# Kernel optimization log

Hardware: AMD Instinct MI355X
Metric: run time of the kernel (lower is better)

## Reference

```python
import jax, jax.numpy as jnp
import numpy as np

B, S, D = 8, 8192, 64
N_HASHES = 8
BUCKET_SIZE = 64
N_BUCKETS = S // BUCKET_SIZE  # 128
SELF_ATTN_VALUE = -5e4  # torch reformer TOKEN_SELF_ATTN_VALUE


def setup_inputs() -> dict:
    key = jax.random.key(0)
    k1, k2, k3 = jax.random.split(key, 3)
    qk = jax.random.normal(k1, (B, S, D), dtype=jnp.float32)
    v = jax.random.normal(k2, (B, S, D), dtype=jnp.float32)
    # LSH random rotations: (dim, n_hashes, n_buckets // 2), shared across batch/heads
    rotations = jax.random.normal(k3, (D, N_HASHES, N_BUCKETS // 2), dtype=jnp.float32)
    return {"qk": qk, "v": v, "rotations": rotations, "query_len": S}


def _look_one_back(x):
    # concatenate each chunk with the preceding chunk (wrapping) along the kv axis
    x_extra = jnp.concatenate([x[:, -1:], x[:, :-1]], axis=1)
    return jnp.concatenate([x, x_extra], axis=2)


def _lsh_bucketed_dots(qk, v, rotations):
    batch, seqlen, dim = qk.shape
    n_buckets = seqlen // BUCKET_SIZE
    # --- hash vectors: rotate, concat with negation, argmax -> bucket ids ---
    rotated = jnp.einsum('btf,fhi->bhti', qk, rotations)           # (B, H, S, nb/2)
    rotated = jnp.concatenate([rotated, -rotated], axis=-1)        # (B, H, S, nb)
    buckets = jnp.argmax(rotated, axis=-1)                         # (B, H, S) int
    offsets = (jnp.arange(N_HASHES) * n_buckets)[None, :, None]    # disjoint per round
    buckets = (buckets + offsets).reshape(batch, -1)               # (B, H*S)

    # --- stable bucket sort via composite key (all keys unique) ---
    ticker = jnp.arange(N_HASHES * seqlen)[None, :]                # (1, H*S)
    buckets_and_t = seqlen * buckets + (ticker % seqlen)
    sticker = jnp.argsort(buckets_and_t, axis=-1)                  # sort permutation
    undo_sort = jnp.argsort(sticker, axis=-1)                      # inverse permutation
    st = sticker % seqlen                                          # original token ids

    # --- gather tokens into bucket order ---
    sqk = jnp.take_along_axis(qk, st[..., None], axis=1)           # (B, H*S, D)
    sv = jnp.take_along_axis(v, st[..., None], axis=1)

    n_chunks = N_HASHES * n_buckets
    bq_t = st.reshape(batch, n_chunks, BUCKET_SIZE)                # (B, C, bs)
    bqk = sqk.reshape(batch, n_chunks, BUCKET_SIZE, dim)
    bv = sv.reshape(batch, n_chunks, BUCKET_SIZE, dim)

    bq = bqk
    bk = bqk / (jnp.linalg.norm(bqk, axis=-1, keepdims=True) + 1e-6)  # unit-length keys

    bk = _look_one_back(bk)       # (B, C, 2*bs, D)
    bv = _look_one_back(bv)
    bkv_t = _look_one_back(bq_t)  # (B, C, 2*bs)

    dots = jnp.einsum('buie,buje->buij', bq, bk) * (dim ** -0.5)   # (B, C, bs, 2*bs)
    self_mask = bq_t[:, :, :, None] == bkv_t[:, :, None, :]
    dots = jnp.where(self_mask, SELF_ATTN_VALUE, dots)
    return dots, undo_sort, bv


def reference(qk, v, rotations, query_len):
    batch, seqlen, dim = qk.shape
    dots, undo_sort, bv = _lsh_bucketed_dots(qk, v, rotations)
    dots_logsumexp = jax.nn.logsumexp(dots, axis=-1, keepdims=True)
    p = jnp.exp(dots - dots_logsumexp)                             # per-bucket softmax
    bo = jnp.einsum('buij,buje->buie', p, bv)                      # (B, C, bs, D)
    so = bo.reshape(batch, -1, dim)                                # (B, H*S, D)
    slogits = dots_logsumexp.reshape(batch, -1)                    # (B, H*S)
    # undo the bucket sort
    o = jnp.take_along_axis(so, undo_sort[..., None], axis=1)
    logits = jnp.take_along_axis(slogits, undo_sort, axis=1)
    o = o.reshape(batch, N_HASHES, seqlen, dim)[:, :, :query_len]
    logits = logits.reshape(batch, N_HASHES, seqlen, 1)[:, :, :query_len]
    # combine across hash rounds, weighted by per-round logsumexp
    probs = jnp.exp(logits - jax.nn.logsumexp(logits, axis=1, keepdims=True))
    out = jnp.sum(o * probs, axis=1)                               # (B, query_len, D)
    return out
```

## Files before the change

kernel.cpp:

```cpp
#include <hip/hip_runtime.h>
#include <math.h>

#define B_  8
#define S_  8192
#define D_  64
#define H_  8
#define NB_ 128
#define NC_ 1024
#define REP_CAP 65536
#define T2_ 2e-3f

typedef _Float16 f16x8 __attribute__((ext_vector_type(8)));
typedef _Float16 f16x2 __attribute__((ext_vector_type(2)));
typedef float    f32x4 __attribute__((ext_vector_type(4)));
typedef unsigned int uint_;

#define MFMA16(A, Bv, C) __builtin_amdgcn_mfma_f32_16x16x32_f16(A, Bv, C, 0, 0, 0)

__global__ __launch_bounds__(256) void rot_prep_kernel(
    const float* __restrict__ rot, _Float16* __restrict__ rotHi,
    _Float16* __restrict__ rotLo, float* __restrict__ rotT,
    int* __restrict__ cnt)
{
  __shared__ float rs[64 * 64];
  const int tid = threadIdx.x, h = blockIdx.x;
  if (h == 0 && tid == 0) *cnt = 0;
#pragma unroll
  for (int it = 0; it < 16; ++it) {
    const int f = it * 4 + (tid >> 6), i = tid & 63;
    rs[f * 64 + i] = rot[f * 512 + h * 64 + i];
  }
  __syncthreads();
  const int i = tid & 63, grp = tid >> 6;
  _Float16 hi[16], lo[16];
  float tf[16];
#pragma unroll
  for (int ff = 0; ff < 16; ++ff) {
    const float x = rs[(grp * 16 + ff) * 64 + i];
    tf[ff] = x;
    hi[ff] = (_Float16)x;
    lo[ff] = (_Float16)(x - (float)hi[ff]);
  }
  f16x8* dH = (f16x8*)(rotHi + h * 4096 + i * 64 + grp * 16);
  f16x8* dL = (f16x8*)(rotLo + h * 4096 + i * 64 + grp * 16);
  dH[0] = ((f16x8*)hi)[0]; dH[1] = ((f16x8*)hi)[1];
  dL[0] = ((f16x8*)lo)[0]; dL[1] = ((f16x8*)lo)[1];
  float4* dT = (float4*)(rotT + h * 4096 + i * 64 + grp * 16);
#pragma unroll
  for (int k = 0; k < 4; ++k) dT[k] = ((float4*)tf)[k];
}

__global__ __launch_bounds__(256) void hash_kernel(
    const float* __restrict__ qk, const float* __restrict__ v,
    const _Float16* __restrict__ rotHi, const _Float16* __restrict__ rotLo,
    _Float16* __restrict__ q16, _Float16* __restrict__ kn16,
    _Float16* __restrict__ v16,
    int* __restrict__ bucket, int* __restrict__ cnt, int2* __restrict__ list)
{
  __shared__ _Float16 rH[64 * 72];
  __shared__ _Float16 rL[64 * 72];
  const int tid  = threadIdx.x;
  const int b    = blockIdx.x & 7;
  const int tile = blockIdx.x >> 3;
  const int lane = tid & 63, w = tid >> 6;
  const int m16  = lane & 15, qd = lane >> 4;

  {
    const int gt = b * S_ + tile * 64 + (tid >> 2);
    const int qu = tid & 3;
    const size_t off = (size_t)gt * 64 + qu * 16;
    float x[16];
#pragma unroll
    for (int k = 0; k < 4; ++k) ((float4*)x)[k] = ((const float4*)(qk + off))[k];
    float ss = 0.f;
#pragma unroll
    for (int k = 0; k < 16; ++k) ss = fmaf(x[k], x[k], ss);
    ss += __shfl_xor(ss, 1); ss += __shfl_xor(ss, 2);
    const float inv = 0.125f / (sqrtf(ss) + 1e-6f);
    f16x8 qh[2], kn[2];
#pragma unroll
    for (int j = 0; j < 16; ++j) {
      qh[j >> 3][j & 7] = (_Float16)x[j];
      kn[j >> 3][j & 7] = (_Float16)(x[j] * inv);
    }
    ((f16x8*)(q16  + off))[0] = qh[0]; ((f16x8*)(q16  + off))[1] = qh[1];
    ((f16x8*)(kn16 + off))[0] = kn[0]; ((f16x8*)(kn16 + off))[1] = kn[1];
    float y[16];
#pragma unroll
    for (int k = 0; k < 4; ++k) ((float4*)y)[k] = ((const float4*)(v + off))[k];
    f16x8 vv[2];
#pragma unroll
    for (int j = 0; j < 16; ++j) vv[j >> 3][j & 7] = (_Float16)y[j];
    ((f16x8*)(v16 + off))[0] = vv[0]; ((f16x8*)(v16 + off))[1] = vv[1];
  }

  const int t = tile * 64 + w * 16 + m16;
  f16x8 BH0, BH1, BL0, BL1;
  {
    const float* src = qk + ((size_t)b * S_ + t) * 64 + 8 * qd;
    float x[16];
    ((float4*)x)[0] = ((const float4*)src)[0];
    ((float4*)x)[1] = ((const float4*)(src + 4))[0];
    ((float4*)x)[2] = ((const float4*)(src + 32))[0];
    ((float4*)x)[3] = ((const float4*)(src + 36))[0];
#pragma unroll
    for (int j = 0; j < 8; ++j) {
      const _Float16 h0 = (_Float16)x[j];
      BH0[j] = h0; BL0[j] = (_Float16)(x[j] - (float)h0);
      const _Float16 h1 = (_Float16)x[j + 8];
      BH1[j] = h1; BL1[j] = (_Float16)(x[j + 8] - (float)h1);
    }
  }
  const int srow = tid >> 2, scol = (tid & 3) * 16;
  const uint_ qd16 = (uint_)(qd << 4);

  f16x8 cH0, cH1, cL0, cL1;
  {
    const _Float16* gH = rotHi + srow * 64 + scol;
    const _Float16* gL = rotLo + srow * 64 + scol;
    cH0 = ((const f16x8*)gH)[0]; cH1 = ((const f16x8*)gH)[1];
    cL0 = ((const f16x8*)gL)[0]; cL1 = ((const f16x8*)gL)[1];
  }

#pragma unroll 1
  for (int h = 0; h < 8; ++h) {
    __syncthreads();
    f16x8 nH0, nH1, nL0, nL1;
    if (h < 7) {
      const _Float16* gH = rotHi + (h + 1) * 4096 + srow * 64 + scol;
      const _Float16* gL = rotLo + (h + 1) * 4096 + srow * 64 + scol;
      nH0 = ((const f16x8*)gH)[0]; nH1 = ((const f16x8*)gH)[1];
      nL0 = ((const f16x8*)gL)[0]; nL1 = ((const f16x8*)gL)[1];
    }
    *(f16x8*)(rH + srow * 72 + scol)     = cH0;
    *(f16x8*)(rH + srow * 72 + scol + 8) = cH1;
    *(f16x8*)(rL + srow * 72 + scol)     = cL0;
    *(f16x8*)(rL + srow * 72 + scol + 8) = cL1;
    __syncthreads();

    f32x4 acc[4];
#pragma unroll
    for (int mt = 0; mt < 4; ++mt) acc[mt] = (f32x4){0.f, 0.f, 0.f, 0.f};
#pragma unroll
    for (int mt = 0; mt < 4; ++mt) {
      const _Float16* aH = rH + (16 * mt + m16) * 72 + 8 * qd;
      const _Float16* aL = rL + (16 * mt + m16) * 72 + 8 * qd;
      const f16x8 AH0 = *(const f16x8*)aH;
      const f16x8 AH1 = *(const f16x8*)(aH + 32);
      const f16x8 AL0 = *(const f16x8*)aL;
      const f16x8 AL1 = *(const f16x8*)(aL + 32);
      acc[mt] = MFMA16(AH0, BH0, acc[mt]);
      acc[mt] = MFMA16(AH1, BH1, acc[mt]);
      acc[mt] = MFMA16(AH0, BL0, acc[mt]);
      acc[mt] = MFMA16(AH1, BL1, acc[mt]);
      acc[mt] = MFMA16(AL0, BH0, acc[mt]);
      acc[mt] = MFMA16(AL1, BH1, acc[mt]);
    }

    float v1M = -1e30f, v2M = -1e30f, v1m = 1e30f, v2m = 1e30f;
#pragma unroll
    for (int mt = 0; mt < 4; ++mt)
#pragma unroll
      for (int rg = 0; rg < 4; ++rg) {
        uint_ u = __float_as_uint(acc[mt][rg]);
        u = (u & 0xFFFFFFC0u) | qd16 | (uint_)((mt << 2) | rg);
        const float xk = __uint_as_float(u);
        v2M = __builtin_amdgcn_fmed3f(v1M, v2M, xk);
        v1M = fmaxf(v1M, xk);
        v2m = __builtin_amdgcn_fmed3f(v1m, v2m, xk);
        v1m = fminf(v1m, xk);
      }
#pragma unroll
    for (int off = 16; off <= 32; off <<= 1) {
      const float o1M = __shfl_xor(v1M, off), o2M = __shfl_xor(v2M, off);
      v2M = __builtin_amdgcn_fmed3f(v1M, o1M, fmaxf(v2M, o2M));
      v1M = fmaxf(v1M, o1M);
      const float o1m = __shfl_xor(v1m, off), o2m = __shfl_xor(v2m, off);
      v2m = __builtin_amdgcn_fmed3f(v1m, o1m, fminf(v2m, o2m));
      v1m = fminf(v1m, o1m);
    }
    if (qd == 0) {
      const uint_ cM = __float_as_uint(v1M) & 63u;
      const uint_ cm = __float_as_uint(v1m) & 63u;
      const int ixM = 16 * (int)((cM >> 2) & 3u) + 4 * (int)(cM >> 4) + (int)(cM & 3u);
      const int ixm = 16 * (int)((cm >> 2) & 3u) + 4 * (int)(cm >> 4) + (int)(cm & 3u);
      const int bkt = (v1M >= -v1m) ? ixM : 64 + ixm;
      bucket[((size_t)(b * 8 + h)) * S_ + t] = bkt;
      const bool flag = ((v1M - v2M) < T2_) | ((v2m - v1m) < T2_) |
                        (fabsf(v1M + v1m) < T2_);
      if (flag) {
        const int s = atomicAdd(cnt, 1);
        if (s < REP_CAP) list[s] = make_int2(b * 8 + h, t);
      }
    }
    cH0 = nH0; cH1 = nH1; cL0 = nL0; cL1 = nL1;
  }
}

__global__ __launch_bounds__(256) void repair_kernel(
    const float* __restrict__ qk, const float* __restrict__ rotT,
    const int* __restrict__ cnt, const int2* __restrict__ list,
    int* __restrict__ bucket)
{
  const int n = min(*cnt, REP_CAP);
  const int lane = threadIdx.x & 63;
  const int wid  = (blockIdx.x * 256 + threadIdx.x) >> 6;
  const int nw   = gridDim.x * 4;
  for (int idx = wid; idx < n; idx += nw) {
    const int bh = list[idx].x, t = list[idx].y;
    const int b = bh >> 3, hh = bh & 7;
    const float* qrow = qk + ((size_t)b * S_ + t) * D_;
    const float* rcol = rotT + hh * 4096 + lane * 64;
    double acc = 0.0;
#pragma unroll
    for (int f0 = 0; f0 < 64; f0 += 4) {
      const float4 rq = *(const float4*)(qrow + f0);
      const float4 rc = *(const float4*)(rcol + f0);
      acc = fma((double)rq.x, (double)rc.x, acc);
      acc = fma((double)rq.y, (double)rc.y, acc);
      acc = fma((double)rq.z, (double)rc.z, acc);
      acc = fma((double)rq.w, (double)rc.w, acc);
    }
    double vM = acc; int iM = lane;
    double vm = acc; int im = lane;
#pragma unroll
    for (int off = 32; off >= 1; off >>= 1) {
      const double voM = __shfl_xor(vM, off); const int ioM = __shfl_xor(iM, off);
      if (voM > vM || (voM == vM && ioM < iM)) { vM = voM; iM = ioM; }
      const double vom = __shfl_xor(vm, off); const int iom = __shfl_xor(im, off);
      if (vom < vm || (vom == vm && iom < im)) { vm = vom; im = iom; }
    }
    if (lane == 0) {
      const int bkt = (vM >= -vm) ? iM : 64 + im;
      bucket[(size_t)bh * S_ + t] = bkt;
    }
  }
}

__global__ __launch_bounds__(1024) void sort_kernel(
    const int* __restrict__ bucket, int* __restrict__ st)
{
  __shared__ uint_ hist32[128 * 67];
  __shared__ unsigned short lb[S_];
  __shared__ int off[128];
  __shared__ int wtot;
  unsigned short* hist16 = (unsigned short*)hist32;
  const int tid = threadIdx.x;
  const int bh  = blockIdx.x;
  const size_t base = (size_t)bh * S_;
  const int lane = tid & 63;
  const unsigned long long ltmask = (1ull << lane) - 1ull;

#pragma unroll
  for (int k = 0; k < 9; ++k) {
    const int i = k * 1024 + tid;
    if (i < 128 * 67) hist32[i] = 0;
  }
  __syncthreads();

  int rl[8];
#pragma unroll
  for (int k = 0; k < 8; ++k) {
    const int t = k * 1024 + tid;
    const int bk = bucket[base + t];
    lb[t] = (unsigned short)bk;
    unsigned long long same = ~0ull;
#pragma unroll
    for (int bit = 0; bit < 7; ++bit) {
      const unsigned long long m = __ballot((bk >> bit) & 1);
      same &= ((bk >> bit) & 1) ? m : ~m;
    }
    rl[k] = __popcll(same & ltmask);
    if ((same & ltmask) == 0ull)
      hist16[bk * 134 + (t >> 6)] = (unsigned short)__popcll(same);
  }
  __syncthreads();

  int s = 0;
  if (tid < 128) {
    const uint_* row = hist32 + tid * 67;
#pragma unroll
    for (int g2 = 0; g2 < 64; ++g2) {
      const uint_ wv = row[g2];
      s += (int)((wv & 0xFFFFu) + (wv >> 16));
    }
  }
  int x = s;
#pragma unroll
  for (int d = 1; d < 64; d <<= 1) {
    const int y = __shfl_up(x, d);
    if (lane >= d) x += y;
  }
  if (tid == 63) wtot = x;
  __syncthreads();
  if (tid < 128) {
    if (tid >= 64) x += wtot;
    off[tid] = x - s;
  }
  __syncthreads();

  if (tid < 128) {
    int run = off[tid];
    unsigned short* rowp = hist16 + tid * 134;
#pragma unroll
    for (int g = 0; g < 128; ++g) {
      const int cg = rowp[g];
      rowp[g] = (unsigned short)run;
      run += cg;
    }
  }
  __syncthreads();

  const int b = bh >> 3, h = bh & 7;
  const size_t stb = (size_t)b * (H_ * S_) + (size_t)h * S_;
#pragma unroll
  for (int k = 0; k < 8; ++k) {
    const int t = k * 1024 + tid;
    const int bk = (int)lb[t];
    const int gb = (int)hist16[bk * 134 + (t >> 6)];
    st[stb + gb + rl[k]] = t;
  }
}

__global__ __launch_bounds__(256, 8) void attn_kernel(
    const _Float16* __restrict__ q16, const _Float16* __restrict__ kn16,
    const _Float16* __restrict__ v16, const int* __restrict__ st,
    _Float16* __restrict__ so, float* __restrict__ slog)
{
  __shared__ _Float16 smem[128 * 72];
  __shared__ __align__(16) int sIds[128];

  const int tid = threadIdx.x;
  const int b   = blockIdx.x & 7;
  const int c   = blockIdx.x >> 3;
  const int cm1 = (c + NC_ - 1) & (NC_ - 1);
  const size_t bst = (size_t)b * (H_ * S_);
  const size_t row0 = bst + (size_t)c * 64;
  const size_t row1 = bst + (size_t)cm1 * 64;

  const int lane = tid & 63;
  const int w    = tid >> 6;
  const int m16  = lane & 15;
  const int qd   = lane >> 4;

  if (tid < 128) sIds[tid] = (tid < 64) ? st[row0 + tid] : st[row1 + tid - 64];

  const int rid = st[row0 + 16 * w + m16];
  f16x8 q0, q1;
  {
    const _Float16* qp = q16 + ((size_t)b * S_ + rid) * 64 + 8 * qd;
    q0 = *(const f16x8*)qp;
    q1 = *(const f16x8*)(qp + 32);
  }

  const int r = tid >> 2, qu = tid & 3;
  {
    const int tokA = st[row0 + r];
    const int tokB = st[row1 + r];
    const f16x8* ska = (const f16x8*)(kn16 + ((size_t)b * S_ + tokA) * 64 + qu * 16);
    const f16x8* skb = (const f16x8*)(kn16 + ((size_t)b * S_ + tokB) * 64 + qu * 16);
    *(f16x8*)(smem + r * 72 + qu * 16)            = ska[0];
    *(f16x8*)(smem + r * 72 + qu * 16 + 8)        = ska[1];
    *(f16x8*)(smem + (64 + r) * 72 + qu * 16)     = skb[0];
    *(f16x8*)(smem + (64 + r) * 72 + qu * 16 + 8) = skb[1];
  }
  __syncthreads();

  f32x4 acc[8];
#pragma unroll
  for (int jt = 0; jt < 8; ++jt) acc[jt] = (f32x4){0.f, 0.f, 0.f, 0.f};

  __builtin_amdgcn_s_setprio(1);
#pragma unroll
  for (int jt = 0; jt < 8; ++jt) {
    const _Float16* krow = smem + (16 * jt + m16) * 72;
    const f16x8 kb0 = *(const f16x8*)(krow + 8 * qd);
    const f16x8 kb1 = *(const f16x8*)(krow + 32 + 8 * qd);
    acc[jt] = MFMA16(kb0, q0, acc[jt]);
    acc[jt] = MFMA16(kb1, q1, acc[jt]);
  }
  __builtin_amdgcn_s_setprio(0);

  float m = -1e30f;
#pragma unroll
  for (int jt = 0; jt < 8; ++jt) {
    const int4 cid = *(const int4*)(sIds + 16 * jt + 4 * qd);
    float x;
    x = acc[jt][0]; if (cid.x == rid) x = -5e4f; acc[jt][0] = x; m = fmaxf(m, x);
    x = acc[jt][1]; if (cid.y == rid) x = -5e4f; acc[jt][1] = x; m = fmaxf(m, x);
    x = acc[jt][2]; if (cid.z == rid) x = -5e4f; acc[jt][2] = x; m = fmaxf(m, x);
    x = acc[jt][3]; if (cid.w == rid) x = -5e4f; acc[jt][3] = x; m = fmaxf(m, x);
  }
  m = fmaxf(m, __shfl_xor(m, 16));
  m = fmaxf(m, __shfl_xor(m, 32));
  float sum = 0.f;
#pragma unroll
  for (int jt = 0; jt < 8; ++jt)
#pragma unroll
    for (int rg = 0; rg < 4; ++rg) {
      const float e = __expf(acc[jt][rg] - m);
      acc[jt][rg] = e;
      sum += e;
    }
  sum += __shfl_xor(sum, 16);
  sum += __shfl_xor(sum, 32);
  const float rinv = 1.f / sum;

  const int hh = c >> 7;
  const size_t hb = ((size_t)(b * 8 + hh)) * S_;
  if (qd == 0) slog[hb + rid] = m + __logf(sum);

  f16x8 pa[4];
#pragma unroll
  for (int s = 0; s < 4; ++s)
#pragma unroll
    for (int j = 0; j < 8; ++j)
      pa[s][j] = (_Float16)acc[2 * s + (j >> 2)][j & 3];

  const int c0 = 2 * r;
  const int k0 = 32 * (c0 >> 5) + 16 * ((c0 >> 2) & 1) + 4 * ((c0 >> 3) & 3) + (c0 & 3);
  const int tok0 = sIds[k0], tok1 = sIds[k0 + 1];
  f16x8 va[2], vb[2];
  {
    const f16x8* s0 = (const f16x8*)(v16 + ((size_t)b * S_ + tok0) * 64 + qu * 16);
    const f16x8* s1 = (const f16x8*)(v16 + ((size_t)b * S_ + tok1) * 64 + qu * 16);
    va[0] = s0[0]; va[1] = s0[1];
    vb[0] = s1[0]; vb[1] = s1[1];
  }
  __syncthreads();

  {
    const int swz = (qu << 3) ^ ((qu & 1) << 5);
    _Float16* dst = smem + (c0 ^ swz);
#pragma unroll
    for (int jj = 0; jj < 16; ++jj) {
      const int d = 16 * qu + jj;
      f16x2 pk; pk[0] = va[jj >> 3][jj & 7]; pk[1] = vb[jj >> 3][jj & 7];
      *(f16x2*)(dst + d * 136) = pk;
    }
  }
  __syncthreads();

  f32x4 oacc[4];
#pragma unroll
  for (int dt = 0; dt < 4; ++dt) oacc[dt] = (f32x4){0.f, 0.f, 0.f, 0.f};
  __builtin_amdgcn_s_setprio(1);
#pragma unroll
  for (int s = 0; s < 4; ++s) {
#pragma unroll
    for (int dt = 0; dt < 4; ++dt) {
      const _Float16* vp = smem + (16 * dt + m16) * 136
                         + 32 * (s ^ (dt & 1)) + 8 * (qd ^ dt);
      const f16x8 bv = *(const f16x8*)(vp);
      oacc[dt] = MFMA16(pa[s], bv, oacc[dt]);
    }
  }
  __builtin_amdgcn_s_setprio(0);

  float rin[4];
#pragma unroll
  for (int rg = 0; rg < 4; ++rg) rin[rg] = __shfl(rinv, 4 * qd + rg);

  __syncthreads();
#pragma unroll
  for (int dt = 0; dt < 4; ++dt)
#pragma unroll
    for (int rg = 0; rg < 4; ++rg)
      smem[(16 * w + 4 * qd + rg) * 72 + 16 * dt + m16] =
          (_Float16)(oacc[dt][rg] * rin[rg]);
  __syncthreads();

  {
    const int tok = sIds[r];
    const f16x8* srcp = (const f16x8*)(smem + r * 72 + qu * 16);
    const f16x8 o0 = srcp[0], o1 = srcp[1];
    f16x8* dstp = (f16x8*)(so + (hb + tok) * 64 + qu * 16);
    dstp[0] = o0; dstp[1] = o1;
  }
}

__global__ __launch_bounds__(256) void combine_kernel(
    const _Float16* __restrict__ so, const float* __restrict__ slog,
    float* __restrict__ out)
{
  const int gid = blockIdx.x * 256 + threadIdx.x;
  const int gt  = gid >> 3;
  const int oct = gid & 7;
  const int b   = gt >> 13;
  const int t   = gt & (S_ - 1);
  const size_t base8 = (size_t)(b * 8) * S_ + t;

  float l[8];
#pragma unroll
  for (int h = 0; h < 8; ++h) l[h] = slog[base8 + (size_t)h * S_];
  float m = l[0];
#pragma unroll
  for (int h = 1; h < 8; ++h) m = fmaxf(m, l[h]);
  float wv[8], W = 0.f;
#pragma unroll
  for (int h = 0; h < 8; ++h) { wv[h] = expf(l[h] - m); W += wv[h]; }
  const float iW = 1.f / W;

  float acc[8] = {0.f, 0.f, 0.f, 0.f, 0.f, 0.f, 0.f, 0.f};
#pragma unroll
  for (int h = 0; h < 8; ++h) {
    const f16x8 vv = *(const f16x8*)(so + (base8 + (size_t)h * S_) * 64 + oct * 8);
#pragma unroll
    for (int j = 0; j < 8; ++j) acc[j] = fmaf(wv[h], (float)vv[j], acc[j]);
  }
  float4 o0, o1;
  o0.x = acc[0] * iW; o0.y = acc[1] * iW; o0.z = acc[2] * iW; o0.w = acc[3] * iW;
  o1.x = acc[4] * iW; o1.y = acc[5] * iW; o1.z = acc[6] * iW; o1.w = acc[7] * iW;
  float4* dst = (float4*)(out + (size_t)gt * 64 + oct * 8);
  dst[0] = o0; dst[1] = o1;
}

extern "C" void kernel_launch(void* const* d_in, const int* in_sizes, int n_in,
                              void* d_out, int out_size, void* d_ws, size_t ws_size,
                              hipStream_t stream)
{
  const float* qk  = (const float*)d_in[0];
  const float* v   = (const float*)d_in[1];
  const float* rot = (const float*)d_in[2];
  float* out = (float*)d_out;

  char* ws = (char*)d_ws;
  const size_t MB = 1ull << 20, KB = 1024;
  int*      bucket = (int*)      (ws + 0 * MB);
  int*      st     = (int*)      (ws + 2 * MB);
  float*    slog   = (float*)    (ws + 4 * MB);
  _Float16* q16    = (_Float16*) (ws + 8 * MB);
  _Float16* kn16   = (_Float16*) (ws + 16 * MB);
  _Float16* v16    = (_Float16*) (ws + 24 * MB);
  _Float16* rotHi  = (_Float16*) (ws + 32 * MB);
  _Float16* rotLo  = (_Float16*) (ws + 32 * MB + 64 * KB);
  int*      cnt    = (int*)      (ws + 32 * MB + 128 * KB);
  int2*     list   = (int2*)     (ws + 32 * MB + 192 * KB);
  float*    rotT   = (float*)    (ws + 32 * MB + 768 * KB);
  _Float16* so     = (_Float16*) (ws + 33 * MB);
  if (ws_size < 98 * MB) return;

  hipLaunchKernelGGL(rot_prep_kernel, dim3(8),         dim3(256),  0, stream,
                     rot, rotHi, rotLo, rotT, cnt);
  hipLaunchKernelGGL(hash_kernel,     dim3(8 * 128),   dim3(256),  0, stream,
                     qk, v, rotHi, rotLo, q16, kn16, v16, bucket, cnt, list);
  hipLaunchKernelGGL(repair_kernel,   dim3(256),       dim3(256),  0, stream,
                     qk, rotT, cnt, list, bucket);
  hipLaunchKernelGGL(sort_kernel,     dim3(64),        dim3(1024), 0, stream,
                     bucket, st);
  hipLaunchKernelGGL(attn_kernel,     dim3(B_ * NC_),  dim3(256),  0, stream,
                     q16, kn16, v16, st, so, slog);
  hipLaunchKernelGGL(combine_kernel,  dim3(B_ * S_ * 8 / 256), dim3(256), 0, stream,
                     so, slog, out);
}
```

Measured before the change: 178.2 us.

## Split bucket sort into parallel histogram and scatter kernels, fuse repair

Replaces the 64-block single-pass sort with a 512-block histogram kernel and a 512-block scatter kernel. Per-slice histograms and packed bucket/rank values go through global workspace, and ghist is zeroed inside hash_kernel. The repair step is folded into the histogram kernel, where each block filters the flagged list for its own (bh, slice), so every block scans the whole list. The aim is to fill the GPU instead of using 64 large blocks. The cost is extra global traffic, redundant list scans and per-block re-scanning of the full histogram. combine_kernel's block-to-token mapping is also changed to interleave batches.

```diff
diff --git a/kernel.cpp b/kernel.cpp
--- a/kernel.cpp
+++ b/kernel.cpp
@@ -55,7 +55,8 @@
     const _Float16* __restrict__ rotHi, const _Float16* __restrict__ rotLo,
     _Float16* __restrict__ q16, _Float16* __restrict__ kn16,
     _Float16* __restrict__ v16,
-    int* __restrict__ bucket, int* __restrict__ cnt, int2* __restrict__ list)
+    int* __restrict__ bucket, int* __restrict__ cnt, int2* __restrict__ list,
+    unsigned short* __restrict__ ghist)
 {
   __shared__ _Float16 rH[64 * 72];
   __shared__ _Float16 rL[64 * 72];
@@ -64,6 +65,9 @@
   const int tile = blockIdx.x >> 3;
   const int lane = tid & 63, w = tid >> 6;
   const int m16  = lane & 15, qd = lane >> 4;
+
+  if (tid < 128)
+    ((int4*)ghist)[(size_t)blockIdx.x * 128 + tid] = make_int4(0, 0, 0, 0);
 
   {
     const int gt = b * S_ + tile * 64 + (tid >> 2);
@@ -197,128 +201,140 @@
   }
 }
 
-__global__ __launch_bounds__(256) void repair_kernel(
+__global__ __launch_bounds__(256) void hist_kernel(
     const float* __restrict__ qk, const float* __restrict__ rotT,
     const int* __restrict__ cnt, const int2* __restrict__ list,
-    int* __restrict__ bucket)
-{
+    int* __restrict__ bucket, unsigned short* __restrict__ ghist,
+    unsigned short* __restrict__ lbr)
+{
+  const int blk = blockIdx.x;
+  const int bh  = blk >> 3;
+  const int sl  = blk & 7;
+  const int tid = threadIdx.x;
+  const int lane = tid & 63, wv = tid >> 6;
+  const unsigned long long ltmask = (1ull << lane) - 1ull;
+
   const int n = min(*cnt, REP_CAP);
-  const int lane = threadIdx.x & 63;
-  const int wid  = (blockIdx.x * 256 + threadIdx.x) >> 6;
-  const int nw   = gridDim.x * 4;
-  for (int idx = wid; idx < n; idx += nw) {
-    const int bh = list[idx].x, t = list[idx].y;
-    const int b = bh >> 3, hh = bh & 7;
-    const float* qrow = qk + ((size_t)b * S_ + t) * D_;
-    const float* rcol = rotT + hh * 4096 + lane * 64;
-    double acc = 0.0;
-#pragma unroll
-    for (int f0 = 0; f0 < 64; f0 += 4) {
-      const float4 rq = *(const float4*)(qrow + f0);
-      const float4 rc = *(const float4*)(rcol + f0);
-      acc = fma((double)rq.x, (double)rc.x, acc);
-      acc = fma((double)rq.y, (double)rc.y, acc);
-      acc = fma((double)rq.z, (double)rc.z, acc);
-      acc = fma((double)rq.w, (double)rc.w, acc);
-    }
-    double vM = acc; int iM = lane;
-    double vm = acc; int im = lane;
-#pragma unroll
-    for (int off = 32; off >= 1; off >>= 1) {
-      const double voM = __shfl_xor(vM, off); const int ioM = __shfl_xor(iM, off);
-      if (voM > vM || (voM == vM && ioM < iM)) { vM = voM; iM = ioM; }
-      const double vom = __shfl_xor(vm, off); const int iom = __shfl_xor(im, off);
-      if (vom < vm || (vom == vm && iom < im)) { vm = vom; im = iom; }
-    }
-    if (lane == 0) {
-      const int bkt = (vM >= -vm) ? iM : 64 + im;
-      bucket[(size_t)bh * S_ + t] = bkt;
-    }
-  }
-}
-
-__global__ __launch_bounds__(1024) void sort_kernel(
-    const int* __restrict__ bucket, int* __restrict__ st)
-{
-  __shared__ uint_ hist32[128 * 67];
-  __shared__ unsigned short lb[S_];
-  __shared__ int off[128];
-  __shared__ int wtot;
-  unsigned short* hist16 = (unsigned short*)hist32;
-  const int tid = threadIdx.x;
-  const int bh  = blockIdx.x;
-  const size_t base = (size_t)bh * S_;
-  const int lane = tid & 63;
-  const unsigned long long ltmask = (1ull << lane) - 1ull;
-
-#pragma unroll
-  for (int k = 0; k < 9; ++k) {
-    const int i = k * 1024 + tid;
-    if (i < 128 * 67) hist32[i] = 0;
-  }
-  __syncthreads();
-
-  int rl[8];
-#pragma unroll
-  for (int k = 0; k < 8; ++k) {
-    const int t = k * 1024 + tid;
-    const int bk = bucket[base + t];
-    lb[t] = (unsigned short)bk;
+  const int b = bh >> 3, hh = bh & 7;
+  for (int c = wv; c * 64 < n; c += 4) {
+    const int idx = c * 64 + lane;
+    int match = 0, ty = 0;
+    if (idx < n) {
+      const int2 e = list[idx];
+      ty = e.y;
+      match = (e.x == bh) & ((e.y >> 10) == sl);
+    }
+    unsigned long long mm = __ballot(match);
+    while (mm) {
+      const int src = (int)__builtin_ctzll(mm); mm &= mm - 1;
+      const int t = __shfl(ty, src);
+      const float* qrow = qk + ((size_t)b * S_ + t) * D_;
+      const float* rcol = rotT + hh * 4096 + lane * 64;
+      double acc = 0.0;
+#pragma unroll
+      for (int f0 = 0; f0 < 64; f0 += 4) {
+        const float4 rq = *(const float4*)(qrow + f0);
+        const float4 rc = *(const float4*)(rcol + f0);
+        acc = fma((double)rq.x, (double)rc.x, acc);
+        acc = fma((double)rq.y, (double)rc.y, acc);
+        acc = fma((double)rq.z, (double)rc.z, acc);
+        acc = fma((double)rq.w, (double)rc.w, acc);
+      }
+      double vM = acc; int iM = lane;
+      double vm = acc; int im = lane;
+#pragma unroll
+      for (int off = 32; off >= 1; off >>= 1) {
+        const double voM = __shfl_xor(vM, off); const int ioM = __shfl_xor(iM, off);
+        if (voM > vM || (voM == vM && ioM < iM)) { vM = voM; iM = ioM; }
+        const double vom = __shfl_xor(vm, off); const int iom = __shfl_xor(im, off);
+        if (vom < vm || (vom == vm && iom < im)) { vm = vom; im = iom; }
+      }
+      if (lane == 0) {
+        const int bkt = (vM >= -vm) ? iM : 64 + im;
+        bucket[(size_t)bh * S_ + t] = bkt;
+      }
+    }
+  }
+  __syncthreads();
+
+  const size_t bb = (size_t)bh * S_;
+  unsigned short* grow = ghist + ((size_t)bh << 14);
+  unsigned short* lrow = lbr + ((size_t)bh << 13);
+#pragma unroll
+  for (int k = 0; k < 4; ++k) {
+    const int t = sl * 1024 + k * 256 + tid;
+    const int bk = bucket[bb + t];
     unsigned long long same = ~0ull;
 #pragma unroll
     for (int bit = 0; bit < 7; ++bit) {
       const unsigned long long m = __ballot((bk >> bit) & 1);
       same &= ((bk >> bit) & 1) ? m : ~m;
     }
-    rl[k] = __popcll(same & ltmask);
+    const int rk = __popcll(same & ltmask);
     if ((same & ltmask) == 0ull)
-      hist16[bk * 134 + (t >> 6)] = (unsigned short)__popcll(same);
-  }
-  __syncthreads();
-
-  int s = 0;
+      grow[bk * 128 + (t >> 6)] = (unsigned short)__popcll(same);
+    lrow[t] = (unsigned short)((bk << 6) | rk);
+  }
+}
+
+__global__ __launch_bounds__(256) void scatter_kernel(
+    const unsigned short* __restrict__ ghist,
+    const unsigned short* __restrict__ lbr, int* __restrict__ st)
+{
+  __shared__ uint_ h32[128 * 64];
+  __shared__ int wtot;
+  unsigned short* h16 = (unsigned short*)h32;
+  const int blk = blockIdx.x;
+  const int bh  = blk >> 3;
+  const int sl  = blk & 7;
+  const int tid = threadIdx.x;
+  const int lane = tid & 63;
+
+  const uint_* gsrc = (const uint_*)(ghist + ((size_t)bh << 14));
+  for (int i = tid; i < 8192; i += 256) h32[i] = gsrc[i];
+  __syncthreads();
+
+  int s = 0, x = 0;
   if (tid < 128) {
-    const uint_* row = hist32 + tid * 67;
+    const uint_* row = h32 + tid * 64;
 #pragma unroll
     for (int g2 = 0; g2 < 64; ++g2) {
       const uint_ wv = row[g2];
       s += (int)((wv & 0xFFFFu) + (wv >> 16));
     }
-  }
-  int x = s;
-#pragma unroll
-  for (int d = 1; d < 64; d <<= 1) {
-    const int y = __shfl_up(x, d);
-    if (lane >= d) x += y;
+    x = s;
+#pragma unroll
+    for (int d = 1; d < 64; d <<= 1) {
+      const int y = __shfl_up(x, d);
+      if (lane >= d) x += y;
+    }
   }
   if (tid == 63) wtot = x;
   __syncthreads();
   if (tid < 128) {
     if (tid >= 64) x += wtot;
-    off[tid] = x - s;
-  }
-  __syncthreads();
-
-  if (tid < 128) {
-    int run = off[tid];
-    unsigned short* rowp = hist16 + tid * 134;
-#pragma unroll
-    for (int g = 0; g < 128; ++g) {
-      const int cg = rowp[g];
-      rowp[g] = (unsigned short)run;
-      run += cg;
+    int run = x - s;
+    uint_* roww = h32 + tid * 64;
+#pragma unroll
+    for (int g2 = 0; g2 < 64; ++g2) {
+      const uint_ wv = roww[g2];
+      const uint_ c0 = wv & 0xFFFFu, c1 = wv >> 16;
+      roww[g2] = (uint_)(run & 0xFFFFu) | ((((uint_)run + c0) & 0xFFFFu) << 16);
+      run += (int)(c0 + c1);
     }
   }
   __syncthreads();
 
   const int b = bh >> 3, h = bh & 7;
   const size_t stb = (size_t)b * (H_ * S_) + (size_t)h * S_;
-#pragma unroll
-  for (int k = 0; k < 8; ++k) {
-    const int t = k * 1024 + tid;
-    const int bk = (int)lb[t];
-    const int gb = (int)hist16[bk * 134 + (t >> 6)];
-    st[stb + gb + rl[k]] = t;
+  const unsigned short* lrow = lbr + ((size_t)bh << 13);
+#pragma unroll
+  for (int k = 0; k < 4; ++k) {
+    const int t = sl * 1024 + k * 256 + tid;
+    const uint_ lr = lrow[t];
+    const int bk = (int)(lr >> 6), rk = (int)(lr & 63u);
+    const int gb = (int)h16[bk * 128 + (t >> 6)];
+    st[stb + gb + rk] = t;
   }
 }
 
@@ -483,11 +499,10 @@
     const _Float16* __restrict__ so, const float* __restrict__ slog,
     float* __restrict__ out)
 {
-  const int gid = blockIdx.x * 256 + threadIdx.x;
-  const int gt  = gid >> 3;
-  const int oct = gid & 7;
-  const int b   = gt >> 13;
-  const int t   = gt & (S_ - 1);
+  const int blk = blockIdx.x;
+  const int b   = blk & 7;
+  const int t   = (blk >> 3) * 32 + (threadIdx.x >> 3);
+  const int oct = threadIdx.x & 7;
   const size_t base8 = (size_t)(b * 8) * S_ + t;
 
   float l[8];
@@ -511,7 +526,7 @@
   float4 o0, o1;
   o0.x = acc[0] * iW; o0.y = acc[1] * iW; o0.z = acc[2] * iW; o0.w = acc[3] * iW;
   o1.x = acc[4] * iW; o1.y = acc[5] * iW; o1.z = acc[6] * iW; o1.w = acc[7] * iW;
-  float4* dst = (float4*)(out + (size_t)gt * 64 + oct * 8);
+  float4* dst = (float4*)(out + ((size_t)b * S_ + t) * 64 + oct * 8);
   dst[0] = o0; dst[1] = o1;
 }
 
@@ -529,6 +544,7 @@
   int*      bucket = (int*)      (ws + 0 * MB);
   int*      st     = (int*)      (ws + 2 * MB);
   float*    slog   = (float*)    (ws + 4 * MB);
+  unsigned short* ghist = (unsigned short*)(ws + 6 * MB);
   _Float16* q16    = (_Float16*) (ws + 8 * MB);
   _Float16* kn16   = (_Float16*) (ws + 16 * MB);
   _Float16* v16    = (_Float16*) (ws + 24 * MB);
@@ -538,17 +554,18 @@
   int2*     list   = (int2*)     (ws + 32 * MB + 192 * KB);
   float*    rotT   = (float*)    (ws + 32 * MB + 768 * KB);
   _Float16* so     = (_Float16*) (ws + 33 * MB);
+  unsigned short* lbr = (unsigned short*)(ws + 97 * MB);
   if (ws_size < 98 * MB) return;
 
-  hipLaunchKernelGGL(rot_prep_kernel, dim3(8),         dim3(256),  0, stream,
+  hipLaunchKernelGGL(rot_prep_kernel, dim3(8),         dim3(256), 0, stream,
                      rot, rotHi, rotLo, rotT, cnt);
-  hipLaunchKernelGGL(hash_kernel,     dim3(8 * 128),   dim3(256),  0, stream,
-                     qk, v, rotHi, rotLo, q16, kn16, v16, bucket, cnt, list);
-  hipLaunchKernelGGL(repair_kernel,   dim3(256),       dim3(256),  0, stream,
-                     qk, rotT, cnt, list, bucket);
-  hipLaunchKernelGGL(sort_kernel,     dim3(64),        dim3(1024), 0, stream,
-                     bucket, st);
-  hipLaunchKernelGGL(attn_kernel,     dim3(B_ * NC_),  dim3(256),  0, stream,
+  hipLaunchKernelGGL(hash_kernel,     dim3(8 * 128),   dim3(256), 0, stream,
+                     qk, v, rotHi, rotLo, q16, kn16, v16, bucket, cnt, list, ghist);
+  hipLaunchKernelGGL(hist_kernel,     dim3(512),       dim3(256), 0, stream,
+                     qk, rotT, cnt, list, bucket, ghist, lbr);
+  hipLaunchKernelGGL(scatter_kernel,  dim3(512),       dim3(256), 0, stream,
+                     ghist, lbr, st);
+  hipLaunchKernelGGL(attn_kernel,     dim3(B_ * NC_),  dim3(256), 0, stream,
                      q16, kn16, v16, st, so, slog);
   hipLaunchKernelGGL(combine_kernel,  dim3(B_ * S_ * 8 / 256), dim3(256), 0, stream,
                      so, slog, out);
```

New measurement: 191.6 us. 1.08x slower.
